# Kernel optimization log

Measured on AMD Instinct MI355X. Metric: run time of the kernel, lower is better.

The kernel has to match this reference:

```python
import jax, jax.numpy as jnp
import numpy as np


def _backwarp(img, flow):
    """Bilinear backward warp of img [B,C,H,W] by flow [B,2,H,W] (pixels).
    Matches torch grid_sample(mode='bilinear', padding_mode='zeros', align_corners=False)
    with the standard softmax-splatting backwarp grid construction."""
    B, C, H, W = img.shape
    # normalized base grid (align_corners=False convention used by backwarp)
    hor = jnp.linspace(-1.0 + 1.0 / W, 1.0 - 1.0 / W, W, dtype=img.dtype)  # [W]
    ver = jnp.linspace(-1.0 + 1.0 / H, 1.0 - 1.0 / H, H, dtype=img.dtype)  # [H]
    gx = hor[None, None, :] + flow[:, 0] / ((W - 1.0) / 2.0)  # [B,H,W]
    gy = ver[None, :, None] + flow[:, 1] / ((H - 1.0) / 2.0)  # [B,H,W]
    # unnormalize (align_corners=False): x = ((g+1)*size - 1)/2
    ix = ((gx + 1.0) * W - 1.0) * 0.5
    iy = ((gy + 1.0) * H - 1.0) * 0.5
    x0 = jnp.floor(ix)
    y0 = jnp.floor(iy)
    wx1 = ix - x0
    wy1 = iy - y0
    wx0 = 1.0 - wx1
    wy0 = 1.0 - wy1

    flat = img.reshape(B, C, H * W)

    def gather(xi, yi):
        valid = (xi >= 0) & (xi <= W - 1) & (yi >= 0) & (yi <= H - 1)  # [B,H,W]
        xc = jnp.clip(xi, 0, W - 1).astype(jnp.int32)
        yc = jnp.clip(yi, 0, H - 1).astype(jnp.int32)
        idx = (yc * W + xc).reshape(B, 1, H * W)
        v = jnp.take_along_axis(flat, jnp.broadcast_to(idx, (B, C, H * W)), axis=2)
        return v.reshape(B, C, H, W) * valid[:, None].astype(img.dtype)

    x1 = x0 + 1.0
    y1 = y0 + 1.0
    out = (gather(x0, y0) * (wy0 * wx0)[:, None]
           + gather(x1, y0) * (wy0 * wx1)[:, None]
           + gather(x0, y1) * (wy1 * wx0)[:, None]
           + gather(x1, y1) * (wy1 * wx1)[:, None])
    return out


def setup_inputs() -> dict:
    key = jax.random.key(0)
    k1, k2, k3 = jax.random.split(key, 3)
    B, C, H, W = 16, 3, 768, 1024
    ten_first = jax.random.normal(k1, (B, C, H, W), dtype=jnp.float32)
    ten_second = jax.random.normal(k2, (B, C, H, W), dtype=jnp.float32)
    tenFlow = jax.random.normal(k3, (B, 2, H, W), dtype=jnp.float32)
    alpha = -jnp.ones((1, 1, 1, 1), dtype=jnp.float32)  # learnable scale, init -1
    return {"ten_first": ten_first, "ten_second": ten_second, "tenFlow": tenFlow, "alpha": alpha}


def reference(ten_first, ten_second, tenFlow, alpha):
    warped = _backwarp(ten_second, tenFlow)
    l1 = jnp.abs(ten_first - warped)                       # [B,C,H,W]
    return alpha * jnp.mean(l1, axis=1, keepdims=True)     # [B,1,H,W]
```

## Files before the change

kernel.cpp:

```cpp
#include <hip/hip_runtime.h>

constexpr int B  = 16;
constexpr int C  = 3;
constexpr int H  = 768;
constexpr int W  = 1024;
constexpr int HW = H * W;

constexpr int TX = 64;
constexpr int TY = 16;
constexpr int R  = 5;
constexpr int TCOLS = TX + 2 * R + 1;
constexpr int TROWS = TY + 2 * R + 1;
constexpr int TSTR  = TCOLS + 1;
constexpr int NXT = W / TX;
constexpr int NYT = H / TY;
constexpr int NWG = B * NXT * NYT;
constexpr int NXCD = 8;
constexpr int PERX = NWG / NXCD;

__global__ __launch_bounds__(256) void warp_l1_mean_tiled(
    const float* __restrict__ first,
    const float* __restrict__ second,
    const float* __restrict__ flow,
    const float* __restrict__ alpha,
    float* __restrict__ out)
{
    __shared__ float tile[C][TROWS][TSTR];

    const int hw  = blockIdx.x;
    const int wid = (hw & (NXCD - 1)) * PERX + (hw >> 3);

    const int b   = wid / (NXT * NYT);
    const int r0  = wid - b * (NXT * NYT);
    const int tyi = r0 / NXT;
    const int txi = r0 - tyi * NXT;

    const int x_base = txi * TX;
    const int y_base = tyi * TY;
    const int x_lo   = x_base - R;
    const int y_lo   = y_base - R;

    const float* __restrict__ sec = second + (size_t)b * C * HW;
    const float* __restrict__ fst = first  + (size_t)b * C * HW;
    const float* __restrict__ fl  = flow   + (size_t)b * 2 * HW;
    float*       __restrict__ op  = out    + (size_t)b * HW;

    for (int j = threadIdx.x; j < TROWS * TCOLS; j += 256) {
        const int r  = j / TCOLS;
        const int cc = j - r * TCOLS;
        const int gx = min(max(x_lo + cc, 0), W - 1);
        const int gy = min(max(y_lo + r,  0), H - 1);
        const int idx = gy * W + gx;
        tile[0][r][cc] = sec[idx];
        tile[1][r][cc] = sec[HW + idx];
        tile[2][r][cc] = sec[2 * HW + idx];
    }
    __syncthreads();

    const int px  = threadIdx.x & 63;
    const int py0 = threadIdx.x >> 6;
    const int x   = x_base + px;
    const float a = alpha[0];

#pragma unroll
    for (int k = 0; k < 4; ++k) {
        const int y = y_base + py0 + 4 * k;
        const int p = y * W + x;

        const float fx = fl[p];
        const float fy = fl[HW + p];

        const float ix = (float)x + fx * ((float)W / (float)(W - 1));
        const float iy = (float)y + fy * ((float)H / (float)(H - 1));

        const float x0f = floorf(ix);
        const float y0f = floorf(iy);
        const float wx1 = ix - x0f;
        const float wy1 = iy - y0f;
        const float wx0 = 1.0f - wx1;
        const float wy0 = 1.0f - wy1;

        const int x0 = (int)x0f;
        const int y0 = (int)y0f;
        const int x1 = x0 + 1;
        const int y1 = y0 + 1;

        const bool vx0 = (x0 >= 0) && (x0 < W);
        const bool vx1 = (x1 >= 0) && (x1 < W);
        const bool vy0 = (y0 >= 0) && (y0 < H);
        const bool vy1 = (y1 >= 0) && (y1 < H);

        const float w00 = wy0 * wx0 * ((vx0 && vy0) ? 1.0f : 0.0f);
        const float w01 = wy0 * wx1 * ((vx1 && vy0) ? 1.0f : 0.0f);
        const float w10 = wy1 * wx0 * ((vx0 && vy1) ? 1.0f : 0.0f);
        const float w11 = wy1 * wx1 * ((vx1 && vy1) ? 1.0f : 0.0f);

        const int lx = x0 - x_lo;
        const int ly = y0 - y_lo;

        float acc = 0.0f;
        if ((unsigned)lx < (unsigned)(TCOLS - 1) &&
            (unsigned)ly < (unsigned)(TROWS - 1)) {
#pragma unroll
            for (int c = 0; c < C; ++c) {
                const float* tp = &tile[c][ly][lx];
                const float v00 = tp[0];
                const float v01 = tp[1];
                const float v10 = tp[TSTR];
                const float v11 = tp[TSTR + 1];
                const float warped = w00 * v00 + w01 * v01 + w10 * v10 + w11 * v11;
                acc += fabsf(fst[c * HW + p] - warped);
            }
        } else {
            const int cx0 = min(max(x0, 0), W - 1);
            const int cx1 = min(max(x1, 0), W - 1);
            const int cy0 = min(max(y0, 0), H - 1);
            const int cy1 = min(max(y1, 0), H - 1);
            const int i00 = cy0 * W + cx0;
            const int i01 = cy0 * W + cx1;
            const int i10 = cy1 * W + cx0;
            const int i11 = cy1 * W + cx1;
#pragma unroll
            for (int c = 0; c < C; ++c) {
                const float* s = sec + c * HW;
                const float warped = w00 * s[i00] + w01 * s[i01]
                                   + w10 * s[i10] + w11 * s[i11];
                acc += fabsf(fst[c * HW + p] - warped);
            }
        }

        op[p] = a * (acc * (1.0f / 3.0f));
    }
}

extern "C" void kernel_launch(void* const* d_in, const int* in_sizes, int n_in,
                              void* d_out, int out_size, void* d_ws, size_t ws_size,
                              hipStream_t stream) {
    const float* first  = (const float*)d_in[0];
    const float* second = (const float*)d_in[1];
    const float* flow   = (const float*)d_in[2];
    const float* alpha  = (const float*)d_in[3];
    float* out = (float*)d_out;

    warp_l1_mean_tiled<<<NWG, 256, 0, stream>>>(first, second, flow, alpha, out);
}
```

Baseline: 392.3 us.

## Vectorize halo tile loads, shrink halo, and prefetch flow and first early

Loads the shared-memory tile of the second image as float4 chunks (19 per row, 77-float row stride), with a clamped scalar fallback only at image borders. The halo radius drops from 5 to 4. The flow and first-image values for each thread's four pixels are now loaded into registers before the tile fill, so their latency overlaps the tile staging. Together these aim to cut global load instructions and exposed memory latency. The cost is more registers, and slightly more samples falling to the slow global-gather path because of the smaller halo.

```diff
diff --git a/kernel.cpp b/kernel.cpp
--- a/kernel.cpp
+++ b/kernel.cpp
@@ -8,10 +8,11 @@
 
 constexpr int TX = 64;
 constexpr int TY = 16;
-constexpr int R  = 5;
+constexpr int R  = 4;
 constexpr int TCOLS = TX + 2 * R + 1;
 constexpr int TROWS = TY + 2 * R + 1;
-constexpr int TSTR  = TCOLS + 1;
+constexpr int CPR   = 19;
+constexpr int TSTR  = 77;
 constexpr int NXT = W / TX;
 constexpr int NYT = H / TY;
 constexpr int NWG = B * NXT * NYT;
@@ -25,7 +26,7 @@
     const float* __restrict__ alpha,
     float* __restrict__ out)
 {
-    __shared__ float tile[C][TROWS][TSTR];
+    __shared__ float tile[C * TROWS * TSTR];
 
     const int hw  = blockIdx.x;
     const int wid = (hw & (NXCD - 1)) * PERX + (hw >> 3);
@@ -45,33 +46,53 @@
     const float* __restrict__ fl  = flow   + (size_t)b * 2 * HW;
     float*       __restrict__ op  = out    + (size_t)b * HW;
 
-    for (int j = threadIdx.x; j < TROWS * TCOLS; j += 256) {
-        const int r  = j / TCOLS;
-        const int cc = j - r * TCOLS;
-        const int gx = min(max(x_lo + cc, 0), W - 1);
-        const int gy = min(max(y_lo + r,  0), H - 1);
-        const int idx = gy * W + gx;
-        tile[0][r][cc] = sec[idx];
-        tile[1][r][cc] = sec[HW + idx];
-        tile[2][r][cc] = sec[2 * HW + idx];
+    const int px  = threadIdx.x & 63;
+    const int py0 = threadIdx.x >> 6;
+    const int x   = x_base + px;
+
+    float pfx[4], pfy[4], pf0[4], pf1[4], pf2[4];
+#pragma unroll
+    for (int k = 0; k < 4; ++k) {
+        const int p = (y_base + py0 + 4 * k) * W + x;
+        pfx[k] = fl[p];
+        pfy[k] = fl[HW + p];
+        pf0[k] = fst[p];
+        pf1[k] = fst[HW + p];
+        pf2[k] = fst[2 * HW + p];
+    }
+
+    for (int j = threadIdx.x; j < C * TROWS * CPR; j += 256) {
+        const int ch  = j / (TROWS * CPR);
+        const int rem = j - ch * (TROWS * CPR);
+        const int r   = rem / CPR;
+        const int q   = rem - r * CPR;
+        const int gy  = y_lo + r;
+        const int gx0 = x_lo + 4 * q;
+        const float* __restrict__ src = sec + (size_t)ch * HW;
+        float4 v;
+        if ((unsigned)gy < (unsigned)H && gx0 >= 0 && gx0 + 3 < W) {
+            v = *reinterpret_cast<const float4*>(src + gy * W + gx0);
+        } else {
+            const int cyW = min(max(gy, 0), H - 1) * W;
+            v.x = src[cyW + min(max(gx0,     0), W - 1)];
+            v.y = src[cyW + min(max(gx0 + 1, 0), W - 1)];
+            v.z = src[cyW + min(max(gx0 + 2, 0), W - 1)];
+            v.w = src[cyW + min(max(gx0 + 3, 0), W - 1)];
+        }
+        float* dst = &tile[(ch * TROWS + r) * TSTR + 4 * q];
+        dst[0] = v.x; dst[1] = v.y; dst[2] = v.z; dst[3] = v.w;
     }
     __syncthreads();
 
-    const int px  = threadIdx.x & 63;
-    const int py0 = threadIdx.x >> 6;
-    const int x   = x_base + px;
-    const float a = alpha[0];
+    const float a3 = alpha[0] * (1.0f / 3.0f);
 
 #pragma unroll
     for (int k = 0; k < 4; ++k) {
         const int y = y_base + py0 + 4 * k;
         const int p = y * W + x;
 
-        const float fx = fl[p];
-        const float fy = fl[HW + p];
-
-        const float ix = (float)x + fx * ((float)W / (float)(W - 1));
-        const float iy = (float)y + fy * ((float)H / (float)(H - 1));
+        const float ix = (float)x + pfx[k] * ((float)W / (float)(W - 1));
+        const float iy = (float)y + pfy[k] * ((float)H / (float)(H - 1));
 
         const float x0f = floorf(ix);
         const float y0f = floorf(iy);
@@ -98,19 +119,16 @@
         const int lx = x0 - x_lo;
         const int ly = y0 - y_lo;
 
-        float acc = 0.0f;
+        float acc;
         if ((unsigned)lx < (unsigned)(TCOLS - 1) &&
             (unsigned)ly < (unsigned)(TROWS - 1)) {
-#pragma unroll
-            for (int c = 0; c < C; ++c) {
-                const float* tp = &tile[c][ly][lx];
-                const float v00 = tp[0];
-                const float v01 = tp[1];
-                const float v10 = tp[TSTR];
-                const float v11 = tp[TSTR + 1];
-                const float warped = w00 * v00 + w01 * v01 + w10 * v10 + w11 * v11;
-                acc += fabsf(fst[c * HW + p] - warped);
-            }
+            const float* tp0 = &tile[(0 * TROWS + ly) * TSTR + lx];
+            const float* tp1 = &tile[(1 * TROWS + ly) * TSTR + lx];
+            const float* tp2 = &tile[(2 * TROWS + ly) * TSTR + lx];
+            const float wa = w00 * tp0[0] + w01 * tp0[1] + w10 * tp0[TSTR] + w11 * tp0[TSTR + 1];
+            const float wb = w00 * tp1[0] + w01 * tp1[1] + w10 * tp1[TSTR] + w11 * tp1[TSTR + 1];
+            const float wc = w00 * tp2[0] + w01 * tp2[1] + w10 * tp2[TSTR] + w11 * tp2[TSTR + 1];
+            acc = fabsf(pf0[k] - wa) + fabsf(pf1[k] - wb) + fabsf(pf2[k] - wc);
         } else {
             const int cx0 = min(max(x0, 0), W - 1);
             const int cx1 = min(max(x1, 0), W - 1);
@@ -120,16 +138,13 @@
             const int i01 = cy0 * W + cx1;
             const int i10 = cy1 * W + cx0;
             const int i11 = cy1 * W + cx1;
-#pragma unroll
-            for (int c = 0; c < C; ++c) {
-                const float* s = sec + c * HW;
-                const float warped = w00 * s[i00] + w01 * s[i01]
-                                   + w10 * s[i10] + w11 * s[i11];
-                acc += fabsf(fst[c * HW + p] - warped);
-            }
+            const float wa = w00 * sec[i00] + w01 * sec[i01] + w10 * sec[i10] + w11 * sec[i11];
+            const float wb = w00 * sec[HW + i00] + w01 * sec[HW + i01] + w10 * sec[HW + i10] + w11 * sec[HW + i11];
+            const float wc = w00 * sec[2*HW + i00] + w01 * sec[2*HW + i01] + w10 * sec[2*HW + i10] + w11 * sec[2*HW + i11];
+            acc = fabsf(pf0[k] - wa) + fabsf(pf1[k] - wb) + fabsf(pf2[k] - wc);
         }
 
-        op[p] = a * (acc * (1.0f / 3.0f));
+        op[p] = a3 * acc;
     }
 }
 
```

Result: faster. 380.7 us (-3.0%).
